# Performance work log

Hardware: AMD Instinct MI355X
Metric: run time of the kernel (lower is better)

Reference implementation:

```python
import jax, jax.numpy as jnp
import numpy as np

N_NODES = 50000
N_EDGES = 1600000
N_GRAPHS = 256
IN_CH = 128
HID = 128
OUT_CH = 10


def gcn_conv(x, W, b, src, dst, ew, num_nodes):
    # PyG GCNConv: add self-loops (weight 1), symmetric deg^-1/2 normalization,
    # linear transform first, aggregate via scatter-add, bias after.
    loop = jnp.arange(num_nodes)
    s = jnp.concatenate([src, loop])
    d = jnp.concatenate([dst, loop])
    w = jnp.concatenate([ew, jnp.ones((num_nodes,), x.dtype)])
    deg = jax.ops.segment_sum(w, d, num_segments=num_nodes)
    dinv = jnp.where(deg > 0, jax.lax.rsqrt(deg), 0.0)
    norm = dinv[s] * dinv[d] * w                     # [E+N]
    h = x @ W                                        # [N, H]
    msg = h[s] * norm[:, None]                       # gather + scale
    out = jax.ops.segment_sum(msg, d, num_segments=num_nodes)  # scatter-add
    return out + b


def setup_inputs() -> dict:
    key = jax.random.key(0)
    ks = jax.random.split(key, 12)
    x = jax.random.normal(ks[0], (N_NODES, IN_CH), jnp.float32)
    edge_index = jax.random.randint(ks[1], (2, N_EDGES), 0, N_NODES, jnp.int64)
    edge_weight = jax.random.uniform(ks[2], (N_EDGES,), jnp.float32)
    batch = jnp.sort(jax.random.randint(ks[3], (N_NODES,), 0, N_GRAPHS, jnp.int64))
    s = 1.0 / np.sqrt(HID)
    W1 = jax.random.normal(ks[4], (IN_CH, HID), jnp.float32) / np.sqrt(IN_CH)
    b1 = jnp.zeros((HID,), jnp.float32)
    W2 = jax.random.normal(ks[5], (HID, HID), jnp.float32) * s
    b2 = jnp.zeros((HID,), jnp.float32)
    W3 = jax.random.normal(ks[6], (HID, HID), jnp.float32) * s
    b3 = jnp.zeros((HID,), jnp.float32)
    lw1 = jax.random.normal(ks[7], (HID, HID), jnp.float32) * s
    lb1 = jax.random.normal(ks[8], (HID,), jnp.float32) * s
    lw2 = jax.random.normal(ks[9], (HID, OUT_CH), jnp.float32) * s
    lb2 = jax.random.normal(ks[10], (OUT_CH,), jnp.float32) * s
    return {"x": x, "edge_index": edge_index, "edge_weight": edge_weight,
            "batch": batch, "W1": W1, "b1": b1, "W2": W2, "b2": b2,
            "W3": W3, "b3": b3, "lw1": lw1, "lb1": lb1, "lw2": lw2, "lb2": lb2}


def reference(x, edge_index, edge_weight, batch, W1, b1, W2, b2, W3, b3, lw1, lb1, lw2, lb2):
    src, dst = edge_index[0], edge_index[1]
    h = jax.nn.relu(gcn_conv(x, W1, b1, src, dst, edge_weight, N_NODES))
    h = jax.nn.relu(gcn_conv(h, W2, b2, src, dst, edge_weight, N_NODES))
    h = gcn_conv(h, W3, b3, src, dst, edge_weight, N_NODES)
    # global mean pool over graphs
    sums = jax.ops.segment_sum(h, batch, num_segments=N_GRAPHS)
    cnt = jax.ops.segment_sum(jnp.ones((N_NODES,), h.dtype), batch, num_segments=N_GRAPHS)
    emb = sums / jnp.maximum(cnt, 1.0)[:, None]      # [G, HID]
    out = (emb @ lw1 + lb1) @ lw2 + lb2              # classify: lin1 -> lin2
    return out
```

## Files before the change

kernel.cpp:

```cpp
#include <hip/hip_runtime.h>

#define N_NODES 50000
#define N_EDGES 1600000
#define N_GRAPHS 256
#define HID 128
#define OUT_CH 10
#define NBUCK 512
#define BNODES ((N_NODES + NBUCK - 1) / NBUCK)
#define BCAP 6144
#define P1BLK 250
#define EPB (N_EDGES / P1BLK)
#define DSENTINEL 127
#define NR 4
#define RSTEP ((N_NODES + NR - 1) / NR)
#define PAD_R 40

typedef __bf16 bf16x8 __attribute__((ext_vector_type(8)));
typedef float f32x4 __attribute__((ext_vector_type(4)));

__device__ inline unsigned bf16rne(float f) {
    unsigned u = __float_as_uint(f);
    return (u + 0x7fffu + ((u >> 16) & 1u)) >> 16;
}

__global__ __launch_bounds__(1024) void bucket_k(const int* __restrict__ src,
                                                 const int* __restrict__ dst,
                                                 const float* __restrict__ ew,
                                                 int* __restrict__ bcount,
                                                 int2* __restrict__ cpair) {
    __shared__ int hist[NBUCK];
    __shared__ int base[NBUCK];
    int t = threadIdx.x;
    for (int i = t; i < NBUCK; i += 1024) hist[i] = 0;
    __syncthreads();
    const int ch0 = blockIdx.x * (EPB / 4);
    const int ch1 = ch0 + (EPB / 4);
    const int4* dst4 = (const int4*)dst;
    for (int ci = ch0 + t; ci < ch1; ci += 1024) {
        int4 d4 = dst4[ci];
        atomicAdd(&hist[d4.x / BNODES], 1);
        atomicAdd(&hist[d4.y / BNODES], 1);
        atomicAdd(&hist[d4.z / BNODES], 1);
        atomicAdd(&hist[d4.w / BNODES], 1);
    }
    __syncthreads();
    for (int i = t; i < NBUCK; i += 1024) {
        int c = hist[i];
        base[i] = (c > 0) ? atomicAdd(&bcount[i], (c + 7) & ~7) : 0;
        hist[i] = 0;
    }
    __syncthreads();
    for (int ci = ch0 + t; ci < ch1; ci += 1024) {
        int4 d4 = dst4[ci];
        int e = ci * 4;
#define PROC(dd, ee)                                              \
        {                                                         \
            int b = (dd) / BNODES;                                \
            int off = base[b] + atomicAdd(&hist[b], 1);           \
            if (off < BCAP) {                                     \
                int2 p;                                           \
                p.x = (((dd) - b * BNODES) << 16) | src[ee];      \
                p.y = __float_as_int(ew[ee]);                     \
                cpair[b * BCAP + off] = p;                        \
            }                                                     \
        }
        PROC(d4.x, e)
        PROC(d4.y, e + 1)
        PROC(d4.z, e + 2)
        PROC(d4.w, e + 3)
#undef PROC
    }
    __syncthreads();
    for (int i = t; i < NBUCK; i += 1024) {
        int c = hist[i];
        int ac = (c + 7) & ~7;
        for (int j = c; j < ac; ++j) {
            int off = base[i] + j;
            if (off < BCAP) {
                int2 p;
                p.x = DSENTINEL << 16;
                p.y = 0;
                cpair[i * BCAP + off] = p;
            }
        }
    }
}

__global__ __launch_bounds__(512) void ell_scatter_k(const int* __restrict__ bcount,
                                                     const int2* __restrict__ cpair,
                                                     int2* __restrict__ ell,
                                                     unsigned* __restrict__ fill4,
                                                     float* __restrict__ dinv) {
    __shared__ int lfill[BNODES * NR];
    __shared__ float wsum[BNODES];
    int b = blockIdx.x;
    int t = threadIdx.x;
    for (int i = t; i < BNODES * NR; i += 512) lfill[i] = 0;
    for (int i = t; i < BNODES; i += 512) wsum[i] = 0.f;
    __syncthreads();
    int cnt = bcount[b];
    if (cnt > BCAP) cnt = BCAP;
    int n0 = b * BNODES;
    int sbase = b * BCAP;
    for (int i = t; i < cnt; i += 512) {
        int2 p = cpair[sbase + i];
        int dloc = p.x >> 16;
        if (dloc < BNODES) {
            int s = p.x & 0xffff;
            int r = s / RSTEP;
            int pos = atomicAdd(&lfill[dloc * NR + r], 1);
            atomicAdd(&wsum[dloc], __int_as_float(p.y));
            if (pos < PAD_R) {
                int2 q;
                q.x = s;
                q.y = p.y;
                ell[((size_t)(n0 + dloc) * NR + r) * PAD_R + pos] = q;
            }
        }
    }
    __syncthreads();
    for (int i = t; i < BNODES; i += 512) {
        int n = n0 + i;
        if (n < N_NODES) {
            unsigned f = 0;
#pragma unroll
            for (int r = 0; r < NR; ++r) {
                int c = lfill[i * NR + r];
                if (c > PAD_R) c = PAD_R;
                f |= (unsigned)c << (8 * r);
            }
            fill4[n] = f;
            dinv[n] = rsqrtf(wsum[i] + 1.0f);
        }
    }
}

__global__ __launch_bounds__(256) void prep_k(const int* __restrict__ batch,
                                              int* __restrict__ gstart,
                                              const float* __restrict__ W1,
                                              const float* __restrict__ W2,
                                              const float* __restrict__ W3,
                                              unsigned short* __restrict__ Wt) {
    int idx = blockIdx.x * 256 + threadIdx.x;
    if (idx < 3 * 16384) {
        int m = idx >> 14;
        int r = idx & 16383;
        const float* W = (m == 0) ? W1 : (m == 1) ? W2 : W3;
        int c = r >> 7, k = r & 127;
        Wt[idx] = (unsigned short)bf16rne(W[k * 128 + c]);
    }
    if (idx < N_NODES) {
        int b = batch[idx];
        int bprev = (idx == 0) ? -1 : batch[idx - 1];
        for (int g = bprev + 1; g <= b; ++g) gstart[g] = idx;
        if (idx == N_NODES - 1) {
            for (int g = b + 1; g <= N_GRAPHS; ++g) gstart[g] = N_NODES;
        }
    }
}

__global__ __launch_bounds__(256) void xconv_k(const float* __restrict__ x,
                                               unsigned short* __restrict__ xb) {
    int i = blockIdx.x * 256 + threadIdx.x;
    if (i >= N_NODES * 16) return;
    const float4* p = (const float4*)x + (size_t)i * 2;
    float4 lo = p[0], hi = p[1];
    uint4 pk;
    pk.x = bf16rne(lo.x) | (bf16rne(lo.y) << 16);
    pk.y = bf16rne(lo.z) | (bf16rne(lo.w) << 16);
    pk.z = bf16rne(hi.x) | (bf16rne(hi.y) << 16);
    pk.w = bf16rne(hi.z) | (bf16rne(hi.w) << 16);
    ((uint4*)xb)[i] = pk;
}

__global__ __launch_bounds__(256, 6) void aggemm_k(const unsigned short* __restrict__ tb,
                                                   const unsigned* __restrict__ fill4,
                                                   const int2* __restrict__ ell,
                                                   const float* __restrict__ dinv,
                                                   const unsigned short* __restrict__ Wt,
                                                   const float* __restrict__ bias,
                                                   unsigned short* __restrict__ outB,
                                                   int relu) {
    __shared__ unsigned short tile[16][136];
    int lane16 = threadIdx.x & 15;
    int local = threadIdx.x >> 4;
    int n = blockIdx.x * 16 + local;
    float dn = dinv[n];
#define UNP(q, f)                                                 \
    float f##0 = __uint_as_float((q).x << 16);                    \
    float f##1 = __uint_as_float((q).x & 0xffff0000u);            \
    float f##2 = __uint_as_float((q).y << 16);                    \
    float f##3 = __uint_as_float((q).y & 0xffff0000u);            \
    float f##4 = __uint_as_float((q).z << 16);                    \
    float f##5 = __uint_as_float((q).z & 0xffff0000u);            \
    float f##6 = __uint_as_float((q).w << 16);                    \
    float f##7 = __uint_as_float((q).w & 0xffff0000u);
    uint4 qs = ((const uint4*)(tb + (size_t)n * 128))[lane16];
    UNP(qs, s)
    float acc0 = s0 * dn, acc1 = s1 * dn, acc2 = s2 * dn, acc3 = s3 * dn;
    float acc4 = s4 * dn, acc5 = s5 * dn, acc6 = s6 * dn, acc7 = s7 * dn;
    unsigned f4 = fill4[n];
#pragma unroll
    for (int r = 0; r < NR; ++r) {
        int c = (f4 >> (8 * r)) & 255;
        const int2* ep = ell + ((size_t)n * NR + r) * PAD_R;
        int i = 0;
        for (; i + 4 <= c; i += 4) {
            int2 p0 = ep[i], p1 = ep[i + 1], p2 = ep[i + 2], p3 = ep[i + 3];
            uint4 q0 = ((const uint4*)(tb + (size_t)p0.x * 128))[lane16];
            uint4 q1 = ((const uint4*)(tb + (size_t)p1.x * 128))[lane16];
            uint4 q2 = ((const uint4*)(tb + (size_t)p2.x * 128))[lane16];
            uint4 q3 = ((const uint4*)(tb + (size_t)p3.x * 128))[lane16];
            float w0 = __int_as_float(p0.y) * dinv[p0.x];
            float w1 = __int_as_float(p1.y) * dinv[p1.x];
            float w2 = __int_as_float(p2.y) * dinv[p2.x];
            float w3 = __int_as_float(p3.y) * dinv[p3.x];
            UNP(q0, a)
            UNP(q1, b)
            UNP(q2, cc)
            UNP(q3, d)
            acc0 += a0 * w0 + b0 * w1 + cc0 * w2 + d0 * w3;
            acc1 += a1 * w0 + b1 * w1 + cc1 * w2 + d1 * w3;
            acc2 += a2 * w0 + b2 * w1 + cc2 * w2 + d2 * w3;
            acc3 += a3 * w0 + b3 * w1 + cc3 * w2 + d3 * w3;
            acc4 += a4 * w0 + b4 * w1 + cc4 * w2 + d4 * w3;
            acc5 += a5 * w0 + b5 * w1 + cc5 * w2 + d5 * w3;
            acc6 += a6 * w0 + b6 * w1 + cc6 * w2 + d6 * w3;
            acc7 += a7 * w0 + b7 * w1 + cc7 * w2 + d7 * w3;
        }
        for (; i < c; ++i) {
            int2 p = ep[i];
            float w = __int_as_float(p.y) * dinv[p.x];
            uint4 q = ((const uint4*)(tb + (size_t)p.x * 128))[lane16];
            UNP(q, a)
            acc0 += a0 * w; acc1 += a1 * w; acc2 += a2 * w; acc3 += a3 * w;
            acc4 += a4 * w; acc5 += a5 * w; acc6 += a6 * w; acc7 += a7 * w;
        }
    }
#undef UNP
    acc0 *= dn; acc1 *= dn; acc2 *= dn; acc3 *= dn;
    acc4 *= dn; acc5 *= dn; acc6 *= dn; acc7 *= dn;
    uint4 pk;
    pk.x = bf16rne(acc0) | (bf16rne(acc1) << 16);
    pk.y = bf16rne(acc2) | (bf16rne(acc3) << 16);
    pk.z = bf16rne(acc4) | (bf16rne(acc5) << 16);
    pk.w = bf16rne(acc6) | (bf16rne(acc7) << 16);
    *(uint4*)&tile[local][lane16 * 8] = pk;
    __syncthreads();

    int wave = threadIdx.x >> 6;
    int lane = threadIdx.x & 63;
    int m = lane & 15;
    int quad = lane >> 4;
    f32x4 acc[2] = {};
#pragma unroll
    for (int kc = 0; kc < 4; ++kc) {
        bf16x8 a = *(const bf16x8*)&tile[m][kc * 32 + quad * 8];
#pragma unroll
        for (int ctl = 0; ctl < 2; ++ctl) {
            int ct = wave * 2 + ctl;
            bf16x8 bfr = *(const bf16x8*)(Wt + (size_t)(ct * 16 + m) * 128 + kc * 32 + quad * 8);
            acc[ctl] = __builtin_amdgcn_mfma_f32_16x16x32_bf16(a, bfr, acc[ctl], 0, 0, 0);
        }
    }
#pragma unroll
    for (int ctl = 0; ctl < 2; ++ctl) {
        int col = (wave * 2 + ctl) * 16 + m;
        float bv = bias[col];
#pragma unroll
        for (int r = 0; r < 4; ++r) {
            int nr = blockIdx.x * 16 + quad * 4 + r;
            float v = acc[ctl][r] + bv;
            if (relu) v = fmaxf(v, 0.f);
            outB[(size_t)nr * 128 + col] = (unsigned short)bf16rne(v);
        }
    }
}

#define PCHUNK 49
__global__ __launch_bounds__(128) void pool1_k(const unsigned short* __restrict__ hb,
                                               const int* __restrict__ batch,
                                               float* __restrict__ pool) {
    int c = threadIdx.x;
    int n0 = blockIdx.x * PCHUNK;
    if (n0 >= N_NODES) return;
    int n1 = n0 + PCHUNK;
    if (n1 > N_NODES) n1 = N_NODES;
    int g = batch[n0];
    float run = 0.f;
    for (int n = n0; n < n1; ++n) {
        int gn = batch[n];
        if (gn != g) {
            atomicAdd(&pool[g * 128 + c], run);
            run = 0.f;
            g = gn;
        }
        run += __uint_as_float((unsigned)hb[(size_t)n * 128 + c] << 16);
    }
    atomicAdd(&pool[g * 128 + c], run);
}

__global__ __launch_bounds__(128) void cls2_k(const float* __restrict__ pool,
                                              const int* __restrict__ gstart,
                                              const float* __restrict__ lw1,
                                              const float* __restrict__ lb1,
                                              const float* __restrict__ lw2,
                                              const float* __restrict__ lb2,
                                              float* __restrict__ out) {
    __shared__ float emb[128];
    __shared__ float mid[128];
    int g = blockIdx.x, c = threadIdx.x;
    float cntf = fmaxf((float)(gstart[g + 1] - gstart[g]), 1.0f);
    emb[c] = pool[(size_t)g * 128 + c] / cntf;
    __syncthreads();
    float a = lb1[c];
    for (int k = 0; k < 128; ++k) a += emb[k] * lw1[k * 128 + c];
    mid[c] = a;
    __syncthreads();
    if (c < OUT_CH) {
        float o = lb2[c];
        for (int k = 0; k < 128; ++k) o += mid[k] * lw2[k * OUT_CH + c];
        out[g * OUT_CH + c] = o;
    }
}

extern "C" void kernel_launch(void* const* d_in, const int* in_sizes, int n_in,
                              void* d_out, int out_size, void* d_ws, size_t ws_size,
                              hipStream_t stream) {
    const float* x = (const float*)d_in[0];
    const int* ei = (const int*)d_in[1];
    const int* src = ei;
    const int* dst = ei + N_EDGES;
    const float* ew = (const float*)d_in[2];
    const int* batch = (const int*)d_in[3];
    const float* W1 = (const float*)d_in[4];
    const float* b1 = (const float*)d_in[5];
    const float* W2 = (const float*)d_in[6];
    const float* b2 = (const float*)d_in[7];
    const float* W3 = (const float*)d_in[8];
    const float* b3 = (const float*)d_in[9];
    const float* lw1 = (const float*)d_in[10];
    const float* lb1 = (const float*)d_in[11];
    const float* lw2 = (const float*)d_in[12];
    const float* lb2 = (const float*)d_in[13];
    float* out = (float*)d_out;

    char* ws = (char*)d_ws;
    size_t off = 0;
    auto alloc = [&](size_t bytes) {
        size_t cur = off;
        off += (bytes + 255) & ~(size_t)255;
        return cur;
    };
    size_t o_bcount = alloc(NBUCK * 4);
    size_t o_pool = alloc(N_GRAPHS * HID * 4);
    size_t zero_end = off;
    size_t o_fill4 = alloc(N_NODES * 4);
    size_t o_dinv = alloc(N_NODES * 4);
    size_t o_gstart = alloc((N_GRAPHS + 1) * 4);
    size_t o_wt = alloc(3 * 16384 * 2);
    size_t o_ell = alloc((size_t)N_NODES * NR * PAD_R * 8);
    size_t o_cpair = alloc((size_t)NBUCK * BCAP * 8);
    size_t o_featA = alloc((size_t)N_NODES * HID * 2);
    size_t o_featB = alloc((size_t)N_NODES * HID * 2);
    (void)ws_size;

    int* bcount = (int*)(ws + o_bcount);
    float* pool = (float*)(ws + o_pool);
    unsigned* fill4 = (unsigned*)(ws + o_fill4);
    float* dinv = (float*)(ws + o_dinv);
    int* gstart = (int*)(ws + o_gstart);
    unsigned short* Wt = (unsigned short*)(ws + o_wt);
    int2* ell = (int2*)(ws + o_ell);
    int2* cpair = (int2*)(ws + o_cpair);
    unsigned short* featA = (unsigned short*)(ws + o_featA);
    unsigned short* featB = (unsigned short*)(ws + o_featB);

    hipMemsetAsync(d_ws, 0, zero_end, stream);

    bucket_k<<<P1BLK, 1024, 0, stream>>>(src, dst, ew, bcount, cpair);
    ell_scatter_k<<<NBUCK, 512, 0, stream>>>(bcount, cpair, ell, fill4, dinv);
    prep_k<<<196, 256, 0, stream>>>(batch, gstart, W1, W2, W3, Wt);
    xconv_k<<<(N_NODES * 16 + 255) / 256, 256, 0, stream>>>(x, featA);

    int agg_blocks = (N_NODES + 15) / 16;
    aggemm_k<<<agg_blocks, 256, 0, stream>>>(featA, fill4, ell, dinv, Wt, b1, featB, 1);
    aggemm_k<<<agg_blocks, 256, 0, stream>>>(featB, fill4, ell, dinv, Wt + 16384, b2, featA, 1);
    aggemm_k<<<agg_blocks, 256, 0, stream>>>(featA, fill4, ell, dinv, Wt + 32768, b3, featB, 0);

    pool1_k<<<(N_NODES + PCHUNK - 1) / PCHUNK, 128, 0, stream>>>(featB, batch, pool);
    cls2_k<<<N_GRAPHS, 128, 0, stream>>>(pool, gstart, lw1, lb1, lw2, lb2, out);
}
```

Before: 358.9 us.

## Flatten ELL rows, pre-fold source dinv into weights, and degree-sort node order

Replaces the four-range padded ELL layout with one flat row per node of capacity 96 (degree capped at 88), built in two passes: a count pass computes per-range offsets, and a fill pass pre-multiplies each edge weight by the source node's dinv. Nodes are counting-sorted by degree into an order array, so each aggregation block handles nodes of similar degree, and the loop processes 8 neighbours per step with zero-padded tails. This removes the per-edge dinv gathers, the range loop overhead and warp divergence from uneven degrees, at the cost of two extra small kernels, scattered output writes, and dropping edges beyond the degree cap. Occupancy hint raised to 8.

Result: slower. 713.9 us (+98.9%).

```diff
diff --git a/kernel.cpp b/kernel.cpp
--- a/kernel.cpp
+++ b/kernel.cpp
@@ -13,7 +13,8 @@
 #define DSENTINEL 127
 #define NR 4
 #define RSTEP ((N_NODES + NR - 1) / NR)
-#define PAD_R 40
+#define PAD_T 96
+#define DEG_CAP 88
 
 typedef __bf16 bf16x8 __attribute__((ext_vector_type(8)));
 typedef float f32x4 __attribute__((ext_vector_type(4)));
@@ -86,17 +87,62 @@
     }
 }
 
-__global__ __launch_bounds__(512) void ell_scatter_k(const int* __restrict__ bcount,
-                                                     const int2* __restrict__ cpair,
-                                                     int2* __restrict__ ell,
-                                                     unsigned* __restrict__ fill4,
-                                                     float* __restrict__ dinv) {
+__global__ __launch_bounds__(512) void ellcount_k(const int* __restrict__ bcount,
+                                                  const int2* __restrict__ cpair,
+                                                  int* __restrict__ loff,
+                                                  int* __restrict__ fill,
+                                                  float* __restrict__ dinv,
+                                                  int* __restrict__ deghist,
+                                                  int2* __restrict__ ell) {
     __shared__ int lfill[BNODES * NR];
     __shared__ float wsum[BNODES];
     int b = blockIdx.x;
     int t = threadIdx.x;
     for (int i = t; i < BNODES * NR; i += 512) lfill[i] = 0;
     for (int i = t; i < BNODES; i += 512) wsum[i] = 0.f;
+    __syncthreads();
+    int cnt = bcount[b];
+    if (cnt > BCAP) cnt = BCAP;
+    int n0 = b * BNODES;
+    int sbase = b * BCAP;
+    for (int i = t; i < cnt; i += 512) {
+        int2 p = cpair[sbase + i];
+        int dloc = p.x >> 16;
+        if (dloc < BNODES) {
+            int s = p.x & 0xffff;
+            atomicAdd(&lfill[dloc * NR + s / RSTEP], 1);
+            atomicAdd(&wsum[dloc], __int_as_float(p.y));
+        }
+    }
+    __syncthreads();
+    for (int i = t; i < BNODES; i += 512) {
+        int n = n0 + i;
+        if (n >= N_NODES) continue;
+        int c0 = lfill[i * NR + 0], c1 = lfill[i * NR + 1];
+        int c2 = lfill[i * NR + 2], c3 = lfill[i * NR + 3];
+        int ct = c0 + c1 + c2 + c3;
+        if (ct > DEG_CAP) ct = DEG_CAP;
+        int* lo = loff + ((size_t)b * BNODES + i) * NR;
+        lo[0] = 0; lo[1] = c0; lo[2] = c0 + c1; lo[3] = c0 + c1 + c2;
+        fill[n] = ct;
+        dinv[n] = rsqrtf(wsum[i] + 1.0f);
+        atomicAdd(&deghist[ct], 1);
+        int cp = (ct + 7) & ~7;
+        int2 z; z.x = 0; z.y = 0;
+        for (int j = ct; j < cp; ++j) ell[(size_t)n * PAD_T + j] = z;
+    }
+}
+
+__global__ __launch_bounds__(512) void ellfill_k(const int* __restrict__ bcount,
+                                                 const int2* __restrict__ cpair,
+                                                 const int* __restrict__ loff,
+                                                 const float* __restrict__ dinv,
+                                                 int2* __restrict__ ell) {
+    __shared__ int lcur[BNODES * NR];
+    int b = blockIdx.x;
+    int t = threadIdx.x;
+    for (int i = t; i < BNODES * NR; i += 512)
+        lcur[i] = loff[(size_t)b * BNODES * NR + i];
     __syncthreads();
     int cnt = bcount[b];
     if (cnt > BCAP) cnt = BCAP;
@@ -108,31 +154,29 @@
         if (dloc < BNODES) {
             int s = p.x & 0xffff;
             int r = s / RSTEP;
-            int pos = atomicAdd(&lfill[dloc * NR + r], 1);
-            atomicAdd(&wsum[dloc], __int_as_float(p.y));
-            if (pos < PAD_R) {
+            int pos = atomicAdd(&lcur[dloc * NR + r], 1);
+            if (pos < DEG_CAP) {
                 int2 q;
                 q.x = s;
-                q.y = p.y;
-                ell[((size_t)(n0 + dloc) * NR + r) * PAD_R + pos] = q;
+                q.y = __float_as_int(__int_as_float(p.y) * dinv[s]);
+                ell[(size_t)(n0 + dloc) * PAD_T + pos] = q;
             }
         }
     }
-    __syncthreads();
-    for (int i = t; i < BNODES; i += 512) {
-        int n = n0 + i;
-        if (n < N_NODES) {
-            unsigned f = 0;
-#pragma unroll
-            for (int r = 0; r < NR; ++r) {
-                int c = lfill[i * NR + r];
-                if (c > PAD_R) c = PAD_R;
-                f |= (unsigned)c << (8 * r);
-            }
-            fill4[n] = f;
-            dinv[n] = rsqrtf(wsum[i] + 1.0f);
-        }
-    }
+}
+
+__global__ __launch_bounds__(128) void dprefix_k(const int* __restrict__ deghist,
+                                                 int* __restrict__ bincur) {
+    __shared__ int h[128];
+    int t = threadIdx.x;
+    h[t] = deghist[t];
+    __syncthreads();
+    if (t == 0) {
+        int s = 0;
+        for (int k = 0; k < 128; ++k) { int v = h[k]; h[k] = s; s += v; }
+    }
+    __syncthreads();
+    bincur[t] = h[t];
 }
 
 __global__ __launch_bounds__(256) void prep_k(const int* __restrict__ batch,
@@ -160,21 +204,31 @@
 }
 
 __global__ __launch_bounds__(256) void xconv_k(const float* __restrict__ x,
-                                               unsigned short* __restrict__ xb) {
+                                               unsigned short* __restrict__ xb,
+                                               const int* __restrict__ fill,
+                                               int* __restrict__ bincur,
+                                               int* __restrict__ order) {
     int i = blockIdx.x * 256 + threadIdx.x;
-    if (i >= N_NODES * 16) return;
-    const float4* p = (const float4*)x + (size_t)i * 2;
-    float4 lo = p[0], hi = p[1];
-    uint4 pk;
-    pk.x = bf16rne(lo.x) | (bf16rne(lo.y) << 16);
-    pk.y = bf16rne(lo.z) | (bf16rne(lo.w) << 16);
-    pk.z = bf16rne(hi.x) | (bf16rne(hi.y) << 16);
-    pk.w = bf16rne(hi.z) | (bf16rne(hi.w) << 16);
-    ((uint4*)xb)[i] = pk;
-}
-
-__global__ __launch_bounds__(256, 6) void aggemm_k(const unsigned short* __restrict__ tb,
-                                                   const unsigned* __restrict__ fill4,
+    if (i < N_NODES * 16) {
+        const float4* p = (const float4*)x + (size_t)i * 2;
+        float4 lo = p[0], hi = p[1];
+        uint4 pk;
+        pk.x = bf16rne(lo.x) | (bf16rne(lo.y) << 16);
+        pk.y = bf16rne(lo.z) | (bf16rne(lo.w) << 16);
+        pk.z = bf16rne(hi.x) | (bf16rne(hi.y) << 16);
+        pk.w = bf16rne(hi.z) | (bf16rne(hi.w) << 16);
+        ((uint4*)xb)[i] = pk;
+    }
+    if (i < N_NODES) {
+        int d = fill[i];
+        int pos = atomicAdd(&bincur[d], 1);
+        order[N_NODES - 1 - pos] = i;
+    }
+}
+
+__global__ __launch_bounds__(256, 8) void aggemm_k(const unsigned short* __restrict__ tb,
+                                                   const int* __restrict__ order,
+                                                   const int* __restrict__ fill,
                                                    const int2* __restrict__ ell,
                                                    const float* __restrict__ dinv,
                                                    const unsigned short* __restrict__ Wt,
@@ -182,10 +236,14 @@
                                                    unsigned short* __restrict__ outB,
                                                    int relu) {
     __shared__ unsigned short tile[16][136];
+    __shared__ int onode[16];
     int lane16 = threadIdx.x & 15;
     int local = threadIdx.x >> 4;
-    int n = blockIdx.x * 16 + local;
+    int n = order[blockIdx.x * 16 + local];
+    if (lane16 == 0) onode[local] = n;
     float dn = dinv[n];
+    int c = fill[n];
+    const uint4* tb4 = (const uint4*)tb;
 #define UNP(q, f)                                                 \
     float f##0 = __uint_as_float((q).x << 16);                    \
     float f##1 = __uint_as_float((q).x & 0xffff0000u);            \
@@ -195,47 +253,46 @@
     float f##5 = __uint_as_float((q).z & 0xffff0000u);            \
     float f##6 = __uint_as_float((q).w << 16);                    \
     float f##7 = __uint_as_float((q).w & 0xffff0000u);
-    uint4 qs = ((const uint4*)(tb + (size_t)n * 128))[lane16];
-    UNP(qs, s)
-    float acc0 = s0 * dn, acc1 = s1 * dn, acc2 = s2 * dn, acc3 = s3 * dn;
-    float acc4 = s4 * dn, acc5 = s5 * dn, acc6 = s6 * dn, acc7 = s7 * dn;
-    unsigned f4 = fill4[n];
-#pragma unroll
-    for (int r = 0; r < NR; ++r) {
-        int c = (f4 >> (8 * r)) & 255;
-        const int2* ep = ell + ((size_t)n * NR + r) * PAD_R;
-        int i = 0;
-        for (; i + 4 <= c; i += 4) {
-            int2 p0 = ep[i], p1 = ep[i + 1], p2 = ep[i + 2], p3 = ep[i + 3];
-            uint4 q0 = ((const uint4*)(tb + (size_t)p0.x * 128))[lane16];
-            uint4 q1 = ((const uint4*)(tb + (size_t)p1.x * 128))[lane16];
-            uint4 q2 = ((const uint4*)(tb + (size_t)p2.x * 128))[lane16];
-            uint4 q3 = ((const uint4*)(tb + (size_t)p3.x * 128))[lane16];
-            float w0 = __int_as_float(p0.y) * dinv[p0.x];
-            float w1 = __int_as_float(p1.y) * dinv[p1.x];
-            float w2 = __int_as_float(p2.y) * dinv[p2.x];
-            float w3 = __int_as_float(p3.y) * dinv[p3.x];
-            UNP(q0, a)
-            UNP(q1, b)
-            UNP(q2, cc)
-            UNP(q3, d)
-            acc0 += a0 * w0 + b0 * w1 + cc0 * w2 + d0 * w3;
-            acc1 += a1 * w0 + b1 * w1 + cc1 * w2 + d1 * w3;
-            acc2 += a2 * w0 + b2 * w1 + cc2 * w2 + d2 * w3;
-            acc3 += a3 * w0 + b3 * w1 + cc3 * w2 + d3 * w3;
-            acc4 += a4 * w0 + b4 * w1 + cc4 * w2 + d4 * w3;
-            acc5 += a5 * w0 + b5 * w1 + cc5 * w2 + d5 * w3;
-            acc6 += a6 * w0 + b6 * w1 + cc6 * w2 + d6 * w3;
-            acc7 += a7 * w0 + b7 * w1 + cc7 * w2 + d7 * w3;
-        }
-        for (; i < c; ++i) {
-            int2 p = ep[i];
-            float w = __int_as_float(p.y) * dinv[p.x];
-            uint4 q = ((const uint4*)(tb + (size_t)p.x * 128))[lane16];
-            UNP(q, a)
-            acc0 += a0 * w; acc1 += a1 * w; acc2 += a2 * w; acc3 += a3 * w;
-            acc4 += a4 * w; acc5 += a5 * w; acc6 += a6 * w; acc7 += a7 * w;
-        }
+    uint4 qs = tb4[(n << 4) + lane16];
+    UNP(qs, S)
+    float acc0 = S0 * dn, acc1 = S1 * dn, acc2 = S2 * dn, acc3 = S3 * dn;
+    float acc4 = S4 * dn, acc5 = S5 * dn, acc6 = S6 * dn, acc7 = S7 * dn;
+    const int4* ep4 = (const int4*)(ell + (size_t)n * PAD_T);
+    int cr = (c + 7) & ~7;
+#pragma unroll 1
+    for (int i = 0; i < cr; i += 8) {
+        int4 ee0 = ep4[(i >> 1) + 0];
+        int4 ee1 = ep4[(i >> 1) + 1];
+        int4 ee2 = ep4[(i >> 1) + 2];
+        int4 ee3 = ep4[(i >> 1) + 3];
+        uint4 q0 = tb4[(ee0.x << 4) + lane16];
+        uint4 q1 = tb4[(ee0.z << 4) + lane16];
+        uint4 q2 = tb4[(ee1.x << 4) + lane16];
+        uint4 q3 = tb4[(ee1.z << 4) + lane16];
+        uint4 q4 = tb4[(ee2.x << 4) + lane16];
+        uint4 q5 = tb4[(ee2.z << 4) + lane16];
+        uint4 q6 = tb4[(ee3.x << 4) + lane16];
+        uint4 q7 = tb4[(ee3.z << 4) + lane16];
+        float w0 = __int_as_float(ee0.y), w1 = __int_as_float(ee0.w);
+        float w2 = __int_as_float(ee1.y), w3 = __int_as_float(ee1.w);
+        float w4 = __int_as_float(ee2.y), w5 = __int_as_float(ee2.w);
+        float w6 = __int_as_float(ee3.y), w7 = __int_as_float(ee3.w);
+        UNP(q0, A)
+        UNP(q1, B)
+        UNP(q2, C)
+        UNP(q3, D)
+        UNP(q4, E)
+        UNP(q5, F)
+        UNP(q6, G)
+        UNP(q7, H)
+        acc0 += A0 * w0 + B0 * w1 + C0 * w2 + D0 * w3 + E0 * w4 + F0 * w5 + G0 * w6 + H0 * w7;
+        acc1 += A1 * w0 + B1 * w1 + C1 * w2 + D1 * w3 + E1 * w4 + F1 * w5 + G1 * w6 + H1 * w7;
+        acc2 += A2 * w0 + B2 * w1 + C2 * w2 + D2 * w3 + E2 * w4 + F2 * w5 + G2 * w6 + H2 * w7;
+        acc3 += A3 * w0 + B3 * w1 + C3 * w2 + D3 * w3 + E3 * w4 + F3 * w5 + G3 * w6 + H3 * w7;
+        acc4 += A4 * w0 + B4 * w1 + C4 * w2 + D4 * w3 + E4 * w4 + F4 * w5 + G4 * w6 + H4 * w7;
+        acc5 += A5 * w0 + B5 * w1 + C5 * w2 + D5 * w3 + E5 * w4 + F5 * w5 + G5 * w6 + H5 * w7;
+        acc6 += A6 * w0 + B6 * w1 + C6 * w2 + D6 * w3 + E6 * w4 + F6 * w5 + G6 * w6 + H6 * w7;
+        acc7 += A7 * w0 + B7 * w1 + C7 * w2 + D7 * w3 + E7 * w4 + F7 * w5 + G7 * w6 + H7 * w7;
     }
 #undef UNP
     acc0 *= dn; acc1 *= dn; acc2 *= dn; acc3 *= dn;
@@ -269,7 +326,7 @@
         float bv = bias[col];
 #pragma unroll
         for (int r = 0; r < 4; ++r) {
-            int nr = blockIdx.x * 16 + quad * 4 + r;
+            int nr = onode[quad * 4 + r];
             float v = acc[ctl][r] + bv;
             if (relu) v = fmaxf(v, 0.f);
             outB[(size_t)nr * 128 + col] = (unsigned short)bf16rne(v);
@@ -354,12 +411,16 @@
     };
     size_t o_bcount = alloc(NBUCK * 4);
     size_t o_pool = alloc(N_GRAPHS * HID * 4);
+    size_t o_deghist = alloc(128 * 4);
     size_t zero_end = off;
-    size_t o_fill4 = alloc(N_NODES * 4);
+    size_t o_bincur = alloc(128 * 4);
+    size_t o_fill = alloc(N_NODES * 4);
     size_t o_dinv = alloc(N_NODES * 4);
+    size_t o_order = alloc(N_NODES * 4);
     size_t o_gstart = alloc((N_GRAPHS + 1) * 4);
     size_t o_wt = alloc(3 * 16384 * 2);
-    size_t o_ell = alloc((size_t)N_NODES * NR * PAD_R * 8);
+    size_t o_loff = alloc((size_t)NBUCK * BNODES * NR * 4);
+    size_t o_ell = alloc((size_t)N_NODES * PAD_T * 8);
     size_t o_cpair = alloc((size_t)NBUCK * BCAP * 8);
     size_t o_featA = alloc((size_t)N_NODES * HID * 2);
     size_t o_featB = alloc((size_t)N_NODES * HID * 2);
@@ -367,10 +428,14 @@
 
     int* bcount = (int*)(ws + o_bcount);
     float* pool = (float*)(ws + o_pool);
-    unsigned* fill4 = (unsigned*)(ws + o_fill4);
+    int* deghist = (int*)(ws + o_deghist);
+    int* bincur = (int*)(ws + o_bincur);
+    int* fill = (int*)(ws + o_fill);
     float* dinv = (float*)(ws + o_dinv);
+    int* order = (int*)(ws + o_order);
     int* gstart = (int*)(ws + o_gstart);
     unsigned short* Wt = (unsigned short*)(ws + o_wt);
+    int* loff = (int*)(ws + o_loff);
     int2* ell = (int2*)(ws + o_ell);
     int2* cpair = (int2*)(ws + o_cpair);
     unsigned short* featA = (unsigned short*)(ws + o_featA);
@@ -379,14 +444,16 @@
     hipMemsetAsync(d_ws, 0, zero_end, stream);
 
     bucket_k<<<P1BLK, 1024, 0, stream>>>(src, dst, ew, bcount, cpair);
-    ell_scatter_k<<<NBUCK, 512, 0, stream>>>(bcount, cpair, ell, fill4, dinv);
+    ellcount_k<<<NBUCK, 512, 0, stream>>>(bcount, cpair, loff, fill, dinv, deghist, ell);
+    ellfill_k<<<NBUCK, 512, 0, stream>>>(bcount, cpair, loff, dinv, ell);
+    dprefix_k<<<1, 128, 0, stream>>>(deghist, bincur);
     prep_k<<<196, 256, 0, stream>>>(batch, gstart, W1, W2, W3, Wt);
-    xconv_k<<<(N_NODES * 16 + 255) / 256, 256, 0, stream>>>(x, featA);
+    xconv_k<<<(N_NODES * 16 + 255) / 256, 256, 0, stream>>>(x, featA, fill, bincur, order);
 
     int agg_blocks = (N_NODES + 15) / 16;
-    aggemm_k<<<agg_blocks, 256, 0, stream>>>(featA, fill4, ell, dinv, Wt, b1, featB, 1);
-    aggemm_k<<<agg_blocks, 256, 0, stream>>>(featB, fill4, ell, dinv, Wt + 16384, b2, featA, 1);
-    aggemm_k<<<agg_blocks, 256, 0, stream>>>(featA, fill4, ell, dinv, Wt + 32768, b3, featB, 0);
+    aggemm_k<<<agg_blocks, 256, 0, stream>>>(featA, order, fill, ell, dinv, Wt, b1, featB, 1);
+    aggemm_k<<<agg_blocks, 256, 0, stream>>>(featB, order, fill, ell, dinv, Wt + 16384, b2, featA, 1);
+    aggemm_k<<<agg_blocks, 256, 0, stream>>>(featA, order, fill, ell, dinv, Wt + 32768, b3, featB, 0);
 
     pool1_k<<<(N_NODES + PCHUNK - 1) / PCHUNK, 128, 0, stream>>>(featB, batch, pool);
     cls2_k<<<N_GRAPHS, 128, 0, stream>>>(pool, gstart, lw1, lb1, lw2, lb2, out);
```

## Pad ELL rows to multiples of four and make aggemm per-wave without block barrier

Applied to the files above, without the earlier changes.

The build step now zero-pads each ELL sub-row up to a multiple of four edges, so the aggregation loop runs only the 4-way unrolled body and the scalar tail is gone. Padding entries point at node 0 with weight zero, which adds a few wasted gathers. The fused GEMM no longer uses __syncthreads: each wave writes its own 4 aggregated rows to a private LDS slice and runs all 8 column tiles of MFMA itself. Only 4 of the 16 MFMA rows are useful, so matrix work per wave rises fourfold, and launch bounds drop from 6 to 4 blocks per SM to make room for the larger accumulator set.

Measured after the change: 435.2 us. +21.3%, slower.

```diff
diff --git a/kernel.cpp b/kernel.cpp
--- a/kernel.cpp
+++ b/kernel.cpp
@@ -123,11 +123,15 @@
         int n = n0 + i;
         if (n < N_NODES) {
             unsigned f = 0;
+            int2 z; z.x = 0; z.y = 0;
 #pragma unroll
             for (int r = 0; r < NR; ++r) {
                 int c = lfill[i * NR + r];
                 if (c > PAD_R) c = PAD_R;
-                f |= (unsigned)c << (8 * r);
+                int cp = (c + 3) & ~3;
+                for (int j = c; j < cp; ++j)
+                    ell[((size_t)n * NR + r) * PAD_R + j] = z;
+                f |= (unsigned)cp << (8 * r);
             }
             fill4[n] = f;
             dinv[n] = rsqrtf(wsum[i] + 1.0f);
@@ -173,7 +177,7 @@
     ((uint4*)xb)[i] = pk;
 }
 
-__global__ __launch_bounds__(256, 6) void aggemm_k(const unsigned short* __restrict__ tb,
+__global__ __launch_bounds__(256, 4) void aggemm_k(const unsigned short* __restrict__ tb,
                                                    const unsigned* __restrict__ fill4,
                                                    const int2* __restrict__ ell,
                                                    const float* __restrict__ dinv,
@@ -181,9 +185,10 @@
                                                    const float* __restrict__ bias,
                                                    unsigned short* __restrict__ outB,
                                                    int relu) {
-    __shared__ unsigned short tile[16][136];
+    __shared__ unsigned short tile[4][4][140];
     int lane16 = threadIdx.x & 15;
     int local = threadIdx.x >> 4;
+    int wave = threadIdx.x >> 6;
     int n = blockIdx.x * 16 + local;
     float dn = dinv[n];
 #define UNP(q, f)                                                 \
@@ -196,16 +201,15 @@
     float f##6 = __uint_as_float((q).w << 16);                    \
     float f##7 = __uint_as_float((q).w & 0xffff0000u);
     uint4 qs = ((const uint4*)(tb + (size_t)n * 128))[lane16];
-    UNP(qs, s)
-    float acc0 = s0 * dn, acc1 = s1 * dn, acc2 = s2 * dn, acc3 = s3 * dn;
-    float acc4 = s4 * dn, acc5 = s5 * dn, acc6 = s6 * dn, acc7 = s7 * dn;
+    UNP(qs, S)
+    float acc0 = S0 * dn, acc1 = S1 * dn, acc2 = S2 * dn, acc3 = S3 * dn;
+    float acc4 = S4 * dn, acc5 = S5 * dn, acc6 = S6 * dn, acc7 = S7 * dn;
     unsigned f4 = fill4[n];
 #pragma unroll
     for (int r = 0; r < NR; ++r) {
         int c = (f4 >> (8 * r)) & 255;
         const int2* ep = ell + ((size_t)n * NR + r) * PAD_R;
-        int i = 0;
-        for (; i + 4 <= c; i += 4) {
+        for (int i = 0; i < c; i += 4) {
             int2 p0 = ep[i], p1 = ep[i + 1], p2 = ep[i + 2], p3 = ep[i + 3];
             uint4 q0 = ((const uint4*)(tb + (size_t)p0.x * 128))[lane16];
             uint4 q1 = ((const uint4*)(tb + (size_t)p1.x * 128))[lane16];
@@ -215,26 +219,18 @@
             float w1 = __int_as_float(p1.y) * dinv[p1.x];
             float w2 = __int_as_float(p2.y) * dinv[p2.x];
             float w3 = __int_as_float(p3.y) * dinv[p3.x];
-            UNP(q0, a)
-            UNP(q1, b)
-            UNP(q2, cc)
-            UNP(q3, d)
-            acc0 += a0 * w0 + b0 * w1 + cc0 * w2 + d0 * w3;
-            acc1 += a1 * w0 + b1 * w1 + cc1 * w2 + d1 * w3;
-            acc2 += a2 * w0 + b2 * w1 + cc2 * w2 + d2 * w3;
-            acc3 += a3 * w0 + b3 * w1 + cc3 * w2 + d3 * w3;
-            acc4 += a4 * w0 + b4 * w1 + cc4 * w2 + d4 * w3;
-            acc5 += a5 * w0 + b5 * w1 + cc5 * w2 + d5 * w3;
-            acc6 += a6 * w0 + b6 * w1 + cc6 * w2 + d6 * w3;
-            acc7 += a7 * w0 + b7 * w1 + cc7 * w2 + d7 * w3;
-        }
-        for (; i < c; ++i) {
-            int2 p = ep[i];
-            float w = __int_as_float(p.y) * dinv[p.x];
-            uint4 q = ((const uint4*)(tb + (size_t)p.x * 128))[lane16];
-            UNP(q, a)
-            acc0 += a0 * w; acc1 += a1 * w; acc2 += a2 * w; acc3 += a3 * w;
-            acc4 += a4 * w; acc5 += a5 * w; acc6 += a6 * w; acc7 += a7 * w;
+            UNP(q0, A)
+            UNP(q1, B)
+            UNP(q2, C)
+            UNP(q3, D)
+            acc0 += A0 * w0 + B0 * w1 + C0 * w2 + D0 * w3;
+            acc1 += A1 * w0 + B1 * w1 + C1 * w2 + D1 * w3;
+            acc2 += A2 * w0 + B2 * w1 + C2 * w2 + D2 * w3;
+            acc3 += A3 * w0 + B3 * w1 + C3 * w2 + D3 * w3;
+            acc4 += A4 * w0 + B4 * w1 + C4 * w2 + D4 * w3;
+            acc5 += A5 * w0 + B5 * w1 + C5 * w2 + D5 * w3;
+            acc6 += A6 * w0 + B6 * w1 + C6 * w2 + D6 * w3;
+            acc7 += A7 * w0 + B7 * w1 + C7 * w2 + D7 * w3;
         }
     }
 #undef UNP
@@ -245,34 +241,31 @@
     pk.y = bf16rne(acc2) | (bf16rne(acc3) << 16);
     pk.z = bf16rne(acc4) | (bf16rne(acc5) << 16);
     pk.w = bf16rne(acc6) | (bf16rne(acc7) << 16);
-    *(uint4*)&tile[local][lane16 * 8] = pk;
-    __syncthreads();
-
-    int wave = threadIdx.x >> 6;
-    int lane = threadIdx.x & 63;
-    int m = lane & 15;
-    int quad = lane >> 4;
-    f32x4 acc[2] = {};
+    *(uint4*)&tile[wave][local & 3][lane16 * 8] = pk;
+
+    int quad = (threadIdx.x >> 4) & 3;
+    int mm = lane16;
+    f32x4 acc[8] = {};
 #pragma unroll
     for (int kc = 0; kc < 4; ++kc) {
-        bf16x8 a = *(const bf16x8*)&tile[m][kc * 32 + quad * 8];
-#pragma unroll
-        for (int ctl = 0; ctl < 2; ++ctl) {
-            int ct = wave * 2 + ctl;
-            bf16x8 bfr = *(const bf16x8*)(Wt + (size_t)(ct * 16 + m) * 128 + kc * 32 + quad * 8);
-            acc[ctl] = __builtin_amdgcn_mfma_f32_16x16x32_bf16(a, bfr, acc[ctl], 0, 0, 0);
-        }
-    }
-#pragma unroll
-    for (int ctl = 0; ctl < 2; ++ctl) {
-        int col = (wave * 2 + ctl) * 16 + m;
-        float bv = bias[col];
-#pragma unroll
-        for (int r = 0; r < 4; ++r) {
-            int nr = blockIdx.x * 16 + quad * 4 + r;
-            float v = acc[ctl][r] + bv;
-            if (relu) v = fmaxf(v, 0.f);
-            outB[(size_t)nr * 128 + col] = (unsigned short)bf16rne(v);
+        bf16x8 a = *(const bf16x8*)&tile[wave][mm & 3][(kc * 4 + quad) * 8];
+#pragma unroll
+        for (int ct = 0; ct < 8; ++ct) {
+            bf16x8 bfr = *(const bf16x8*)(Wt + (size_t)(ct * 16 + mm) * 128 + kc * 32 + quad * 8);
+            acc[ct] = __builtin_amdgcn_mfma_f32_16x16x32_bf16(a, bfr, acc[ct], 0, 0, 0);
+        }
+    }
+    if (quad == 0) {
+        int nb = blockIdx.x * 16 + wave * 4;
+#pragma unroll
+        for (int ct = 0; ct < 8; ++ct) {
+            float bv = bias[ct * 16 + mm];
+#pragma unroll
+            for (int r = 0; r < 4; ++r) {
+                float v = acc[ct][r] + bv;
+                if (relu) v = fmaxf(v, 0.f);
+                outB[(size_t)(nb + r) * 128 + ct * 16 + mm] = (unsigned short)bf16rne(v);
+            }
         }
     }
 }
```
